# Optimization experiments

Measured on AMD Instinct MI355X. Metric: run time of the kernel, lower is better.

## Reference

```python
import jax, jax.numpy as jnp
import numpy as np

VOCAB, D, H = 30522, 768, 128
B, S = 32, 1024
N_SENT, SENT_LEN = 16, 64


def _lstm_dir(x, W_ih, W_hh, b, reverse=False):
    """Single-direction LSTM, PyTorch gate order (i,f,g,o). x: [B,T,D] -> [B,T,H]."""
    pre = jnp.einsum('btd,gd->btg', x, W_ih) + b  # [B,T,4H]
    if reverse:
        pre = pre[:, ::-1]
    nb = x.shape[0]
    h0 = jnp.zeros((nb, H), x.dtype)

    def step(carry, xt):
        h, c = carry
        g = xt + h @ W_hh.T
        i, f, gg, o = jnp.split(g, 4, axis=-1)
        c = jax.nn.sigmoid(f) * c + jax.nn.sigmoid(i) * jnp.tanh(gg)
        h = jax.nn.sigmoid(o) * jnp.tanh(c)
        return (h, c), h

    _, hs = jax.lax.scan(step, (h0, h0), jnp.swapaxes(pre, 0, 1))
    hs = jnp.swapaxes(hs, 0, 1)  # [B,T,H]
    if reverse:
        hs = hs[:, ::-1]
    return hs


def _bilstm(x, Wf, Uf, bf, Wb, Ub, bb):
    return jnp.concatenate([_lstm_dir(x, Wf, Uf, bf, False),
                            _lstm_dir(x, Wb, Ub, bb, True)], axis=-1)


def setup_inputs() -> dict:
    key = jax.random.key(0)
    ks = jax.random.split(key, 20)
    p = lambda i, shape: (jax.random.normal(ks[i], shape, dtype=jnp.float32) * 0.05)
    inp = {
        'word_inputs': jax.random.randint(ks[0], (B, S), 0, VOCAB, dtype=jnp.int32),
        'sent_tokens': jax.random.randint(ks[1], (B, N_SENT, SENT_LEN), 0, VOCAB, dtype=jnp.int32),
        'seq_len': S,
        'E': p(2, (VOCAB, D)),
        'lstm_Wih_f': p(3, (4 * H, D)), 'lstm_Whh_f': p(4, (4 * H, H)), 'lstm_b_f': p(5, (4 * H,)),
        'lstm_Wih_b': p(6, (4 * H, D)), 'lstm_Whh_b': p(7, (4 * H, H)), 'lstm_b_b': p(8, (4 * H,)),
        'sent_Wih_f': p(9, (4 * H, D)), 'sent_Whh_f': p(10, (4 * H, H)), 'sent_b_f': p(11, (4 * H,)),
        'sent_Wih_b': p(12, (4 * H, D)), 'sent_Whh_b': p(13, (4 * H, H)), 'sent_b_b': p(14, (4 * H,)),
        'gate_W': p(15, (2 * H, 4 * H)), 'gate_b': p(16, (2 * H,)),
    }
    return inp


def reference(word_inputs, sent_tokens, seq_len, E,
              lstm_Wih_f, lstm_Whh_f, lstm_b_f, lstm_Wih_b, lstm_Whh_b, lstm_b_b,
              sent_Wih_f, sent_Whh_f, sent_b_f, sent_Wih_b, sent_Whh_b, sent_b_b,
              gate_W, gate_b):
    # wordrep: embedding lookup (full-length sequences, all-ones masks)
    word_rep = E[word_inputs]  # [B,S,D]
    feature_out = _bilstm(word_rep, lstm_Wih_f, lstm_Whh_f, lstm_b_f,
                          lstm_Wih_b, lstm_Whh_b, lstm_b_b)  # [B,S,2H]

    # per-sentence BiLSTM: each sentence has its own fresh hidden state, so
    # the original python loop over sentences == batched BiLSTM over (B*N, L)
    st = sent_tokens.reshape(B * N_SENT, SENT_LEN)
    sent_rep = E[st]  # [B*N, L, D]
    sent_out = _bilstm(sent_rep, sent_Wih_f, sent_Whh_f, sent_b_f,
                       sent_Wih_b, sent_Whh_b, sent_b_b)  # [B*N, L, 2H]
    feature_out_sents = sent_out.reshape(B, N_SENT * SENT_LEN, 2 * H)  # [B,S,2H]

    gamma = jax.nn.sigmoid(
        jnp.concatenate([feature_out, feature_out_sents], axis=-1) @ gate_W.T + gate_b)
    return gamma * feature_out + (1.0 - gamma) * feature_out_sents
```

## Files before the change

kernel.cpp:

```cpp
#include <hip/hip_runtime.h>

typedef unsigned short u16;
typedef __attribute__((ext_vector_type(8))) short short8;
typedef __attribute__((ext_vector_type(4))) float f32x4;

__device__ __forceinline__ u16 f2b(float f){
    unsigned u = __builtin_bit_cast(unsigned, f);
    u += 0x7fffu + ((u >> 16) & 1u);
    return (u16)(u >> 16);
}
__device__ __forceinline__ float b2f(u16 s){
    unsigned u = ((unsigned)s) << 16;
    return __builtin_bit_cast(float, u);
}
__device__ __forceinline__ float sigm(float x){ return 1.f/(1.f + __expf(-x)); }
__device__ __forceinline__ float tanhf2(float x){
    float e = __expf(2.f * x);
    return 1.f - 2.f/(1.f + e);
}

__global__ __launch_bounds__(256) void cvt_bf16(const float* __restrict__ s,
                                                u16* __restrict__ d, int n4){
    int i = blockIdx.x*256 + threadIdx.x;
    if (i < n4){
        float4 v = ((const float4*)s)[i];
        ushort4 o;
        o.x = f2b(v.x); o.y = f2b(v.y); o.z = f2b(v.z); o.w = f2b(v.w);
        ((ushort4*)d)[i] = o;
    }
}

__global__ __launch_bounds__(192) void cvt_wih_perm(const float* __restrict__ s,
                                                    u16* __restrict__ d){
    int r = blockIdx.x;
    int j = threadIdx.x;
    int g = r >> 7, u = r & 127;
    int ro = u * 4 + g;
    float4 v = ((const float4*)(s + (size_t)r * 768))[j];
    ushort4 o;
    o.x = f2b(v.x); o.y = f2b(v.y); o.z = f2b(v.z); o.w = f2b(v.w);
    ((ushort4*)(d + (size_t)ro * 768))[j] = o;
}

__global__ __launch_bounds__(256) void cvt_whh_perm(const float* __restrict__ s,
                                                    u16* __restrict__ d){
    int idx = blockIdx.x*256 + threadIdx.x;
    if (idx >= 512*32) return;
    int r = idx >> 5, j = idx & 31;
    int g = r >> 7, u = r & 127;
    int ro = u * 4 + g;
    float4 v = ((const float4*)(s + (size_t)r * 128))[j];
    ushort4 o;
    o.x = f2b(v.x); o.y = f2b(v.y); o.z = f2b(v.z); o.w = f2b(v.w);
    ((ushort4*)(d + (size_t)ro * 128))[j] = o;
}

__global__ __launch_bounds__(256) void gemm_embed(
    const u16* __restrict__ E, const int* __restrict__ tok,
    const u16* __restrict__ Wt, const float* __restrict__ bf_,
    const float* __restrict__ bb_, u16* __restrict__ pre, int sentMode)
{
    __shared__ __align__(16) u16 Asm[128*32];
    __shared__ __align__(16) u16 Bsm[128*32];
    const int m0 = blockIdx.x * 128, n0 = blockIdx.y * 128;
    const int tid = threadIdx.x;
    const int ar = tid >> 2, ch = (tid & 3) * 8;
    const u16* ap0 = E + (size_t)tok[m0 + ar] * 768 + ch;
    const u16* ap1 = E + (size_t)tok[m0 + 64 + ar] * 768 + ch;
    const u16* bp0 = Wt + (size_t)(n0 + ar) * 768 + ch;
    const u16* bp1 = Wt + (size_t)(n0 + 64 + ar) * 768 + ch;
    const int lane = tid & 63, wave = tid >> 6;
    const int wm = (wave >> 1) * 64, wn = (wave & 1) * 64;
    const int qr = lane >> 4, lr = lane & 15;
    f32x4 acc[4][4] = {};
    for (int k0 = 0; k0 < 768; k0 += 32){
        __syncthreads();
        *(short8*)&Asm[ar*32 + ch]      = *(const short8*)(ap0 + k0);
        *(short8*)&Asm[(64+ar)*32 + ch] = *(const short8*)(ap1 + k0);
        *(short8*)&Bsm[ar*32 + ch]      = *(const short8*)(bp0 + k0);
        *(short8*)&Bsm[(64+ar)*32 + ch] = *(const short8*)(bp1 + k0);
        __syncthreads();
        short8 af[4], bfr[4];
        #pragma unroll
        for (int i = 0; i < 4; ++i){
            af[i]  = *(const short8*)&Asm[(wm + i*16 + lr)*32 + qr*8];
            bfr[i] = *(const short8*)&Bsm[(wn + i*16 + lr)*32 + qr*8];
        }
        #pragma unroll
        for (int i = 0; i < 4; ++i)
            #pragma unroll
            for (int j = 0; j < 4; ++j)
                acc[i][j] = __builtin_amdgcn_mfma_f32_16x16x32_bf16(af[i], bfr[j], acc[i][j], 0, 0, 0);
    }
    #pragma unroll
    for (int j = 0; j < 4; ++j){
        int col = n0 + wn + j*16 + lr;
        int dirO = col >> 9, pcol = col & 511;
        int uu = pcol >> 2, gg = pcol & 3;
        float bias = (dirO ? bb_ : bf_)[gg*128 + uu];
        int wL = uu >> 4, uL = uu & 15;
        int tidPart = wL*64 + (uL & 3)*16 + (uL & 12);
        #pragma unroll
        for (int i = 0; i < 4; ++i){
            #pragma unroll
            for (int r = 0; r < 4; ++r){
                int mrow = m0 + wm + i*16 + qr*4 + r;
                int blk, t, cL, Tdim;
                if (sentMode){ int s = mrow >> 6;  t = mrow & 63;   blk = (dirO<<7) + (s >> 2); cL = s & 3; Tdim = 64; }
                else         { int b = mrow >> 10; t = mrow & 1023; blk = (dirO<<3) + (b >> 2); cL = b & 3; Tdim = 1024; }
                size_t idx = (((size_t)blk * Tdim + t) * 512 + (tidPart + cL)) * 4 + gg;
                pre[idx] = f2b(acc[i][j][r] + bias);
            }
        }
    }
}

__global__ __launch_bounds__(512)
__attribute__((amdgpu_waves_per_eu(2)))
void lstm_rec(
    const u16* __restrict__ preW, const u16* __restrict__ preS,
    const u16* __restrict__ Whp,
    float* __restrict__ fo, float* __restrict__ fs)
{
    const int bg = blockIdx.x;
    const u16* preBlk; const u16* wh; float* out;
    int T, dir, grpb;
    if (bg < 16){
        dir = bg >> 3; grpb = bg & 7; T = 1024;
        preBlk = preW + (size_t)bg * 1024 * 2048;
        wh = Whp + (size_t)dir*512*128; out = fo;
    } else {
        int sg = bg - 16; dir = sg >> 7; grpb = sg & 127; T = 64;
        preBlk = preS + (size_t)sg * 64 * 2048;
        wh = Whp + (size_t)(2+dir)*512*128; out = fs;
    }
    const int tid  = threadIdx.x;
    const int w    = tid >> 6, lane = tid & 63;
    const int lr = lane & 15, qr = lane >> 4;
    const int t0 = dir ? (T-1) : 0;
    const int dt = dir ? -1 : 1;

    short8 aw[4][4];
    #pragma unroll
    for (int i = 0; i < 4; ++i)
        #pragma unroll
        for (int kk = 0; kk < 4; ++kk)
            asm volatile("global_load_dwordx4 %0, %1, off"
                         : "=v"(aw[i][kk])
                         : "v"(wh + (size_t)(w*64 + i*16 + lr)*128 + kk*32 + qr*8));
    asm volatile("s_waitcnt vmcnt(0)");
    __builtin_amdgcn_sched_barrier(0);

    __shared__ __align__(16) u16 hb[2][512];
    for (int k = tid; k < 1024; k += 512) ((u16*)hb)[k] = 0;

    const int cL = lr & 3;
    const int u  = w*16 + (lr >> 2)*4 + qr;
    const int hbW   = cL*128 + (u ^ (cL << 4));
    const int rbase = cL*128;
    const int rxor  = cL << 4;
    const bool s2 = (lr & 4) != 0, s3 = (lr & 8) != 0;

    const int chainG = grpb*4 + cL;
    float* po = out + ((size_t)chainG*T + t0)*256 + dir*128 + u;
    const long ostep = (long)dt * 256;

    const long pstep = (long)dt * 2048;
    const u16* p = preBlk + (long)t0 * 2048 + tid*4;
    ushort4 buf[4];
    buf[0] = *(const ushort4*)p;
    buf[1] = *(const ushort4*)(p + pstep);
    buf[2] = *(const ushort4*)(p + 2*pstep);
    p += 3*pstep;

    float cst = 0.f;
    __syncthreads();

#define LSTM_STEP(J, LOADJ) do {                                              \
    short8 bfr[4];                                                            \
    _Pragma("unroll")                                                         \
    for (int kk = 0; kk < 4; ++kk)                                            \
        bfr[kk] = *(const short8*)&hb[(J)&1][rbase + ((kk*32 + qr*8) ^ rxor)];\
    buf[LOADJ] = *(const ushort4*)p;                                          \
    p += pstep;                                                               \
    f32x4 a0 = {}, a1 = {}, a2 = {}, a3 = {};                                 \
    _Pragma("unroll")                                                         \
    for (int kk = 0; kk < 4; ++kk){                                           \
        a0 = __builtin_amdgcn_mfma_f32_16x16x32_bf16(aw[0][kk], bfr[kk], a0, 0, 0, 0); \
        a1 = __builtin_amdgcn_mfma_f32_16x16x32_bf16(aw[1][kk], bfr[kk], a1, 0, 0, 0); \
        a2 = __builtin_amdgcn_mfma_f32_16x16x32_bf16(aw[2][kk], bfr[kk], a2, 0, 0, 0); \
        a3 = __builtin_amdgcn_mfma_f32_16x16x32_bf16(aw[3][kk], bfr[kk], a3, 0, 0, 0); \
    }                                                                         \
    float m0 = s3 ? (s2 ? a3[0] : a2[0]) : (s2 ? a1[0] : a0[0]);              \
    float m1 = s3 ? (s2 ? a3[1] : a2[1]) : (s2 ? a1[1] : a0[1]);              \
    float m2 = s3 ? (s2 ? a3[2] : a2[2]) : (s2 ? a1[2] : a0[2]);              \
    float m3 = s3 ? (s2 ? a3[3] : a2[3]) : (s2 ? a1[3] : a0[3]);              \
    ushort4 pc = buf[J];                                                      \
    float g0 = b2f(pc.x) + m0, g1 = b2f(pc.y) + m1;                           \
    float g2 = b2f(pc.z) + m2, g3 = b2f(pc.w) + m3;                           \
    float gi = sigm(g0), gf = sigm(g1);                                       \
    float gg = tanhf2(g2), go = sigm(g3);                                     \
    float c = gf*cst + gi*gg; cst = c;                                        \
    float h = go*tanhf2(c);                                                   \
    po[0] = h;                                                                \
    po += ostep;                                                              \
    hb[((J)&1)^1][hbW] = f2b(h);                                              \
    __builtin_amdgcn_sched_barrier(0);                                        \
    asm volatile("s_waitcnt lgkmcnt(0)");                                     \
    __builtin_amdgcn_s_barrier();                                             \
    __builtin_amdgcn_sched_barrier(0);                                        \
} while(0)

    for (int itBase = 0; itBase < T; itBase += 4){
        LSTM_STEP(0, 3);
        LSTM_STEP(1, 0);
        LSTM_STEP(2, 1);
        LSTM_STEP(3, 2);
    }
#undef LSTM_STEP
}

__global__ __launch_bounds__(256) void gemm_gate(
    const u16* __restrict__ gW, const float* __restrict__ gb,
    const float* __restrict__ fo, const float* __restrict__ fs,
    float* __restrict__ out)
{
    __shared__ __align__(16) u16 Asm[128*32];
    __shared__ __align__(16) u16 Bsm[128*32];
    const int m0 = blockIdx.x * 128, n0 = blockIdx.y * 128;
    const int tid = threadIdx.x;
    const int ar = tid >> 2, ch = (tid & 3) * 8;
    const float* af0 = fo + (size_t)(m0 + ar) * 256 + ch;
    const float* af1 = fo + (size_t)(m0 + 64 + ar) * 256 + ch;
    const float* as0 = fs + (size_t)(m0 + ar) * 256 + ch;
    const float* as1 = fs + (size_t)(m0 + 64 + ar) * 256 + ch;
    const u16* bp0 = gW + (size_t)(n0 + ar) * 512 + ch;
    const u16* bp1 = gW + (size_t)(n0 + 64 + ar) * 512 + ch;
    const int lane = tid & 63, wave = tid >> 6;
    const int wm = (wave >> 1) * 64, wn = (wave & 1) * 64;
    const int qr = lane >> 4, lr = lane & 15;
    f32x4 acc[4][4] = {};
    for (int k0 = 0; k0 < 512; k0 += 32){
        __syncthreads();
        const float* s0 = (k0 < 256) ? (af0 + k0) : (as0 + (k0 - 256));
        const float* s1 = (k0 < 256) ? (af1 + k0) : (as1 + (k0 - 256));
        float4 x0 = ((const float4*)s0)[0], x1 = ((const float4*)s0)[1];
        float4 y0 = ((const float4*)s1)[0], y1 = ((const float4*)s1)[1];
        ushort4 a0; a0.x=f2b(x0.x); a0.y=f2b(x0.y); a0.z=f2b(x0.z); a0.w=f2b(x0.w);
        ushort4 a1; a1.x=f2b(x1.x); a1.y=f2b(x1.y); a1.z=f2b(x1.z); a1.w=f2b(x1.w);
        ushort4 b0; b0.x=f2b(y0.x); b0.y=f2b(y0.y); b0.z=f2b(y0.z); b0.w=f2b(y0.w);
        ushort4 b1; b1.x=f2b(y1.x); b1.y=f2b(y1.y); b1.z=f2b(y1.z); b1.w=f2b(y1.w);
        *(ushort4*)&Asm[ar*32 + ch]          = a0;
        *(ushort4*)&Asm[ar*32 + ch + 4]      = a1;
        *(ushort4*)&Asm[(64+ar)*32 + ch]     = b0;
        *(ushort4*)&Asm[(64+ar)*32 + ch + 4] = b1;
        *(short8*)&Bsm[ar*32 + ch]      = *(const short8*)(bp0 + k0);
        *(short8*)&Bsm[(64+ar)*32 + ch] = *(const short8*)(bp1 + k0);
        __syncthreads();
        short8 af[4], bfr[4];
        #pragma unroll
        for (int i = 0; i < 4; ++i){
            af[i]  = *(const short8*)&Asm[(wm + i*16 + lr)*32 + qr*8];
            bfr[i] = *(const short8*)&Bsm[(wn + i*16 + lr)*32 + qr*8];
        }
        #pragma unroll
        for (int i = 0; i < 4; ++i)
            #pragma unroll
            for (int j = 0; j < 4; ++j)
                acc[i][j] = __builtin_amdgcn_mfma_f32_16x16x32_bf16(af[i], bfr[j], acc[i][j], 0, 0, 0);
    }
    #pragma unroll
    for (int j = 0; j < 4; ++j){
        int col = n0 + wn + j*16 + lr;
        float bias = gb[col];
        #pragma unroll
        for (int i = 0; i < 4; ++i){
            #pragma unroll
            for (int r = 0; r < 4; ++r){
                int row = m0 + wm + i*16 + qr*4 + r;
                size_t o = (size_t)row*256 + col;
                float gamma = sigm(acc[i][j][r] + bias);
                out[o] = gamma * fo[o] + (1.f - gamma) * fs[o];
            }
        }
    }
}

extern "C" void kernel_launch(void* const* d_in, const int* in_sizes, int n_in,
                              void* d_out, int out_size, void* d_ws, size_t ws_size,
                              hipStream_t stream)
{
    (void)in_sizes; (void)n_in; (void)out_size; (void)ws_size;
    const int*   wordTok = (const int*)d_in[0];
    const int*   sentTok = (const int*)d_in[1];
    const float* E       = (const float*)d_in[3];
    const float* WihWf   = (const float*)d_in[4];
    const float* WhhWf   = (const float*)d_in[5];
    const float* bWf     = (const float*)d_in[6];
    const float* WihWb   = (const float*)d_in[7];
    const float* WhhWb   = (const float*)d_in[8];
    const float* bWb     = (const float*)d_in[9];
    const float* WihSf   = (const float*)d_in[10];
    const float* WhhSf   = (const float*)d_in[11];
    const float* bSf     = (const float*)d_in[12];
    const float* WihSb   = (const float*)d_in[13];
    const float* WhhSb   = (const float*)d_in[14];
    const float* bSb     = (const float*)d_in[15];
    const float* gateW   = (const float*)d_in[16];
    const float* gateB   = (const float*)d_in[17];
    float* out = (float*)d_out;

    char* w = (char*)d_ws;
    u16* Eb   = (u16*)w;  w += (size_t)30522*768*2;
    u16* Ww   = (u16*)w;  w += (size_t)1024*768*2;
    u16* Ws_  = (u16*)w;  w += (size_t)1024*768*2;
    u16* gWb  = (u16*)w;  w += (size_t)256*512*2;
    u16* preW = (u16*)w;  w += (size_t)32768*1024*2;
    u16* preS = (u16*)w;  w += (size_t)32768*1024*2;
    float* fo = (float*)w; w += (size_t)32768*256*4;
    float* fs = (float*)w; w += (size_t)32768*256*4;
    u16* Whp  = (u16*)w;  w += (size_t)4*512*128*2;

    const int nE4 = 30522*768/4;
    cvt_bf16<<<(nE4+255)/256, 256, 0, stream>>>(E, Eb, nE4);
    cvt_wih_perm<<<512, 192, 0, stream>>>(WihWf, Ww);
    cvt_wih_perm<<<512, 192, 0, stream>>>(WihWb, Ww + 512*768);
    cvt_wih_perm<<<512, 192, 0, stream>>>(WihSf, Ws_);
    cvt_wih_perm<<<512, 192, 0, stream>>>(WihSb, Ws_ + 512*768);
    const int nG4 = 256*512/4;
    cvt_bf16<<<(nG4+255)/256, 256, 0, stream>>>(gateW, gWb, nG4);
    cvt_whh_perm<<<64, 256, 0, stream>>>(WhhWf, Whp);
    cvt_whh_perm<<<64, 256, 0, stream>>>(WhhWb, Whp + 512*128);
    cvt_whh_perm<<<64, 256, 0, stream>>>(WhhSf, Whp + 2*512*128);
    cvt_whh_perm<<<64, 256, 0, stream>>>(WhhSb, Whp + 3*512*128);

    gemm_embed<<<dim3(256,8), 256, 0, stream>>>(Eb, wordTok, Ww, bWf, bWb, preW, 0);
    gemm_embed<<<dim3(256,8), 256, 0, stream>>>(Eb, sentTok, Ws_, bSf, bSb, preS, 1);
    lstm_rec<<<272, 512, 0, stream>>>(preW, preS, Whp, fo, fs);
    gemm_gate<<<dim3(256,2), 256, 0, stream>>>(gWb, gateB, fo, fs, out);
}
```

Before: 1.095 ms.

## Pack two timesteps of gate preactivations per thread into 16-byte loads

The input-projection GEMM now writes preactivations so that each thread's gates for two consecutive timesteps are interleaved, with the pair order flipped for the reverse direction. The recurrent kernel issues one 16-byte load per two steps instead of an 8-byte load every step, and prefetches four pairs deep (eight steps). The sched_barrier masks are relaxed to 0x77 so the compiler may move some instruction types across the barrier. This trades fewer, wider global loads on the serial recurrence for more live registers and a changed producer layout.

```diff
diff --git a/kernel.cpp b/kernel.cpp
--- a/kernel.cpp
+++ b/kernel.cpp
@@ -108,7 +108,8 @@
                 int blk, t, cL, Tdim;
                 if (sentMode){ int s = mrow >> 6;  t = mrow & 63;   blk = (dirO<<7) + (s >> 2); cL = s & 3; Tdim = 64; }
                 else         { int b = mrow >> 10; t = mrow & 1023; blk = (dirO<<3) + (b >> 2); cL = b & 3; Tdim = 1024; }
-                size_t idx = (((size_t)blk * Tdim + t) * 512 + (tidPart + cL)) * 4 + gg;
+                size_t idx = (((size_t)blk * (Tdim >> 1) + (t >> 1)) * 512 + (tidPart + cL)) * 8
+                           + (((t & 1) ^ dirO) << 2) + gg;
                 pre[idx] = f2b(acc[i][j][r] + bias);
             }
         }
@@ -127,11 +128,11 @@
     int T, dir, grpb;
     if (bg < 16){
         dir = bg >> 3; grpb = bg & 7; T = 1024;
-        preBlk = preW + (size_t)bg * 1024 * 2048;
+        preBlk = preW + (size_t)bg * 512 * 4096;
         wh = Whp + (size_t)dir*512*128; out = fo;
     } else {
         int sg = bg - 16; dir = sg >> 7; grpb = sg & 127; T = 64;
-        preBlk = preS + (size_t)sg * 64 * 2048;
+        preBlk = preS + (size_t)sg * 32 * 4096;
         wh = Whp + (size_t)(2+dir)*512*128; out = fs;
     }
     const int tid  = threadIdx.x;
@@ -165,24 +166,28 @@
     float* po = out + ((size_t)chainG*T + t0)*256 + dir*128 + u;
     const long ostep = (long)dt * 256;
 
-    const long pstep = (long)dt * 2048;
-    const u16* p = preBlk + (long)t0 * 2048 + tid*4;
-    ushort4 buf[4];
-    buf[0] = *(const ushort4*)p;
-    buf[1] = *(const ushort4*)(p + pstep);
-    buf[2] = *(const ushort4*)(p + 2*pstep);
-    p += 3*pstep;
+    const int  t0pair = dir ? (T/2 - 1) : 0;
+    const long ppstep = (long)dt * 4096;
+    const u16* pp = preBlk + (long)t0pair * 4096 + tid*8;
+    short8 buf[4];
+    buf[0] = *(const short8*)pp;
+    buf[1] = *(const short8*)(pp + ppstep);
+    buf[2] = *(const short8*)(pp + 2*ppstep);
+    buf[3] = *(const short8*)(pp + 3*ppstep);
+    pp += 4*ppstep;
 
     float cst = 0.f;
     __syncthreads();
 
-#define LSTM_STEP(J, LOADJ) do {                                              \
+#define LSTM_STEP(J, SLOT, HALF, DOLOAD) do {                                 \
     short8 bfr[4];                                                            \
     _Pragma("unroll")                                                         \
     for (int kk = 0; kk < 4; ++kk)                                            \
         bfr[kk] = *(const short8*)&hb[(J)&1][rbase + ((kk*32 + qr*8) ^ rxor)];\
-    buf[LOADJ] = *(const ushort4*)p;                                          \
-    p += pstep;                                                               \
+    ushort4 pc;                                                               \
+    pc.x = (u16)buf[SLOT][(HALF)*4+0]; pc.y = (u16)buf[SLOT][(HALF)*4+1];     \
+    pc.z = (u16)buf[SLOT][(HALF)*4+2]; pc.w = (u16)buf[SLOT][(HALF)*4+3];     \
+    if (DOLOAD){ buf[SLOT] = *(const short8*)pp; pp += ppstep; }              \
     f32x4 a0 = {}, a1 = {}, a2 = {}, a3 = {};                                 \
     _Pragma("unroll")                                                         \
     for (int kk = 0; kk < 4; ++kk){                                           \
@@ -195,7 +200,6 @@
     float m1 = s3 ? (s2 ? a3[1] : a2[1]) : (s2 ? a1[1] : a0[1]);              \
     float m2 = s3 ? (s2 ? a3[2] : a2[2]) : (s2 ? a1[2] : a0[2]);              \
     float m3 = s3 ? (s2 ? a3[3] : a2[3]) : (s2 ? a1[3] : a0[3]);              \
-    ushort4 pc = buf[J];                                                      \
     float g0 = b2f(pc.x) + m0, g1 = b2f(pc.y) + m1;                           \
     float g2 = b2f(pc.z) + m2, g3 = b2f(pc.w) + m3;                           \
     float gi = sigm(g0), gf = sigm(g1);                                       \
@@ -205,17 +209,21 @@
     po[0] = h;                                                                \
     po += ostep;                                                              \
     hb[((J)&1)^1][hbW] = f2b(h);                                              \
-    __builtin_amdgcn_sched_barrier(0);                                        \
+    __builtin_amdgcn_sched_barrier(0x77);                                     \
     asm volatile("s_waitcnt lgkmcnt(0)");                                     \
     __builtin_amdgcn_s_barrier();                                             \
-    __builtin_amdgcn_sched_barrier(0);                                        \
+    __builtin_amdgcn_sched_barrier(0x77);                                     \
 } while(0)
 
-    for (int itBase = 0; itBase < T; itBase += 4){
-        LSTM_STEP(0, 3);
-        LSTM_STEP(1, 0);
-        LSTM_STEP(2, 1);
-        LSTM_STEP(3, 2);
+    for (int itBase = 0; itBase < T; itBase += 8){
+        LSTM_STEP(0, 0, 0, 0);
+        LSTM_STEP(1, 0, 1, 1);
+        LSTM_STEP(2, 1, 0, 0);
+        LSTM_STEP(3, 1, 1, 1);
+        LSTM_STEP(4, 2, 0, 0);
+        LSTM_STEP(5, 2, 1, 1);
+        LSTM_STEP(6, 3, 0, 0);
+        LSTM_STEP(7, 3, 1, 1);
     }
 #undef LSTM_STEP
 }
```

Result: faster. 1.065 ms (-2.7%).
